# Kernel tuning notes

Hardware: AMD Instinct MI355X
Metric: run time of the kernel (lower is better)

The kernel has to match this reference:

```python
import jax, jax.numpy as jnp
import numpy as np

LN_EPS = 1e-5


def setup_inputs() -> dict:
    key = jax.random.key(0)
    k1, = jax.random.split(key, 1)
    B, C, H, W = 16, 512, 64, 64
    HW = H * W
    x = jax.random.normal(k1, (B, C, H, W), dtype=jnp.float32)
    gamma = jnp.ones((), dtype=jnp.float32)          # Scale(1) learnable scalar
    ln_weight = jnp.ones((HW,), dtype=jnp.float32)   # LayerNorm weight
    ln_bias = jnp.zeros((HW,), dtype=jnp.float32)    # LayerNorm bias
    return {"x": x, "gamma": gamma, "ln_weight": ln_weight, "ln_bias": ln_bias}


def reference(x, gamma, ln_weight, ln_bias):
    B, C, H, W = x.shape
    v = x.reshape(B, C, H * W)                       # [B, C, HW] (Q = K = V)
    energy = jnp.einsum('bcn,bdn->bcd', v, v)        # [B, C, C]
    attn = jax.nn.softmax(energy, axis=-1)
    out = jnp.einsum('bcd,bdn->bcn', attn, v)        # [B, C, HW]
    out = gamma * out + v                            # scale + residual
    # LayerNorm over last dim (HW), torch eps=1e-5
    mean = jnp.mean(out, axis=-1, keepdims=True)
    var = jnp.mean(jnp.square(out - mean), axis=-1, keepdims=True)
    out = (out - mean) * jax.lax.rsqrt(var + LN_EPS) * ln_weight + ln_bias
    return out.reshape(B, C, H, W)
```

## Files before the change

### kernel.cpp

```cpp
#include <hip/hip_runtime.h>
#include <hip/hip_bf16.h>

#define B_DIM 16
#define C_DIM 512
#define HW_DIM 4096
#define LN_EPS 1e-5f

using bf16 = __hip_bfloat16;
typedef __bf16 v8bf __attribute__((ext_vector_type(8)));
typedef float v4f __attribute__((ext_vector_type(4)));
typedef unsigned short v8us __attribute__((ext_vector_type(8)));
typedef unsigned short v4us __attribute__((ext_vector_type(4)));
using gptr_t = const __attribute__((address_space(1))) void*;
using lptr_t = __attribute__((address_space(3))) void*;

__device__ __forceinline__ unsigned short f2bf(float f) {
  unsigned int u = __float_as_uint(f);
  u = (u + 0x7fffu + ((u >> 16) & 1u)) >> 16;
  return (unsigned short)u;
}
__device__ __forceinline__ float bf2f(unsigned short us) {
  return __uint_as_float(((unsigned int)us) << 16);
}

__global__ __launch_bounds__(256) void k_convert_transpose(
    const float* __restrict__ x, unsigned short* __restrict__ v,
    unsigned short* __restrict__ vt) {
  __shared__ unsigned short tile[64 * 64];
  const int tid = threadIdx.x;
  const int b = blockIdx.z;
  const int n0 = blockIdx.x * 64;
  const int c0 = blockIdx.y * 64;
  const size_t boff = (size_t)b * ((size_t)C_DIM * HW_DIM);
  const float* xb = x + boff;
  unsigned short* vb = v + boff;
  unsigned short* vtb = vt + boff;

  const int cl = tid >> 3;
  const int hb = tid & 7;
  const int h8 = hb * 8;
#pragma unroll
  for (int j = 0; j < 2; ++j) {
    const int c = cl + j * 32;
    const float* src = xb + (size_t)(c0 + c) * HW_DIM + n0 + h8;
    const float4 f0 = ((const float4*)src)[0];
    const float4 f1 = ((const float4*)src)[1];
    v8us pack;
    pack[0] = f2bf(f0.x); pack[1] = f2bf(f0.y);
    pack[2] = f2bf(f0.z); pack[3] = f2bf(f0.w);
    pack[4] = f2bf(f1.x); pack[5] = f2bf(f1.y);
    pack[6] = f2bf(f1.z); pack[7] = f2bf(f1.w);
    *(v8us*)(vb + (size_t)(c0 + c) * HW_DIM + n0 + h8) = pack;
    const int key = (c & 7) ^ ((c >> 3) & 7);
    *(v8us*)(tile + c * 64 + ((hb ^ key) << 3)) = pack;
  }
  __syncthreads();
  const int nl = tid >> 3;
  const int c8 = (tid & 7) * 8;
  const int n = 2 * nl;
  v8us pa, pb;
#pragma unroll
  for (int e = 0; e < 8; ++e) {
    const int r = c8 + e;
    const int key = (r & 7) ^ ((r >> 3) & 7);
    const unsigned int w = *(const unsigned int*)(
        tile + r * 64 + (((n >> 3) ^ key) << 3) + (n & 7));
    pa[e] = (unsigned short)(w & 0xffffu);
    pb[e] = (unsigned short)(w >> 16);
  }
  *(v8us*)(vtb + (size_t)(n0 + n) * C_DIM + c0 + c8) = pa;
  *(v8us*)(vtb + (size_t)(n0 + n + 1) * C_DIM + c0 + c8) = pb;
}

__device__ __forceinline__ void stage_tiles(
    const bf16* __restrict__ a_base, const bf16* __restrict__ b_base,
    const int stride, const int k0, const int wave, const int lane,
    bf16* ldsA, bf16* ldsB) {
  const int srow = lane >> 3;
  const int skcol = (lane & 7) * 8;
#pragma unroll
  for (int i = 0; i < 4; ++i) {
    const int ci = wave * 4 + i;
    const int row = ci * 8 + srow;
    __builtin_amdgcn_global_load_lds(
        (gptr_t)(a_base + (size_t)row * stride + k0 + skcol),
        (lptr_t)(ldsA + ci * 512), 16, 0, 0);
    __builtin_amdgcn_global_load_lds(
        (gptr_t)(b_base + (size_t)row * stride + k0 + skcol),
        (lptr_t)(ldsB + ci * 512), 16, 0, 0);
  }
}

__device__ __forceinline__ void compute_tile(
    const bf16* ldsA, const bf16* ldsB, const int wave, const int lane,
    v4f acc[4][4]) {
  const int kb = (lane >> 4) * 8;
  const int rl = lane & 15;
  const int wr = wave >> 1, wc = wave & 1;
#pragma unroll
  for (int kk = 0; kk < 2; ++kk) {
    v8bf af[4], bfr[4];
#pragma unroll
    for (int m = 0; m < 4; ++m)
      af[m] = *(const v8bf*)(ldsA + (wr * 64 + m * 16 + rl) * 64 + kk * 32 + kb);
#pragma unroll
    for (int n = 0; n < 4; ++n)
      bfr[n] = *(const v8bf*)(ldsB + (wc * 64 + n * 16 + rl) * 64 + kk * 32 + kb);
#pragma unroll
    for (int m = 0; m < 4; ++m)
#pragma unroll
      for (int n = 0; n < 4; ++n)
        acc[m][n] = __builtin_amdgcn_mfma_f32_16x16x32_bf16(af[m], bfr[n], acc[m][n], 0, 0, 0);
  }
}

__device__ __forceinline__ void gemm_dbuf_loop(
    const bf16* __restrict__ a_base, const bf16* __restrict__ b_base,
    const int stride, const int ksteps, const int wave, const int lane,
    bf16* ldsA0, bf16* ldsB0, bf16* ldsA1, bf16* ldsB1, v4f acc[4][4]) {
  stage_tiles(a_base, b_base, stride, 0, wave, lane, ldsA0, ldsB0);
  __syncthreads();
  int cur = 0;
  for (int kt = 0; kt < ksteps - 1; ++kt) {
    if (cur == 0)
      stage_tiles(a_base, b_base, stride, (kt + 1) * 64, wave, lane, ldsA1, ldsB1);
    else
      stage_tiles(a_base, b_base, stride, (kt + 1) * 64, wave, lane, ldsA0, ldsB0);
    compute_tile(cur == 0 ? ldsA0 : ldsA1, cur == 0 ? ldsB0 : ldsB1, wave, lane, acc);
    __syncthreads();
    cur ^= 1;
  }
  compute_tile(cur == 0 ? ldsA0 : ldsA1, cur == 0 ? ldsB0 : ldsB1, wave, lane, acc);
}

__global__ __launch_bounds__(256) void k_gemm1(
    const bf16* __restrict__ v, float* __restrict__ e_part) {
  __shared__ __align__(16) bf16 lds[4][128 * 64];
  int t = blockIdx.x;
  const int ks = t >> 8;
  t &= 255;
  const int b = t >> 4;
  const int cb = (t >> 2) & 3;
  const int db = t & 3;
  const int tid = threadIdx.x;
  const int wave = tid >> 6, lane = tid & 63;
  const bf16* vb = v + (size_t)b * ((size_t)C_DIM * HW_DIM) + ks * (HW_DIM / 2);
  v4f acc[4][4] = {};
  gemm_dbuf_loop(vb + (size_t)(cb * 128) * HW_DIM,
                 vb + (size_t)(db * 128) * HW_DIM,
                 HW_DIM, (HW_DIM / 2) / 64, wave, lane,
                 lds[0], lds[1], lds[2], lds[3], acc);
  float* eb = e_part + (size_t)ks * ((size_t)B_DIM * C_DIM * C_DIM) +
              (size_t)b * (C_DIM * C_DIM);
  const int wr = wave >> 1, wc = wave & 1;
  const int rl = lane & 15;
  const int r0 = (lane >> 4) * 4;
#pragma unroll
  for (int m = 0; m < 4; ++m)
#pragma unroll
    for (int n = 0; n < 4; ++n) {
      const int row0 = cb * 128 + wr * 64 + m * 16 + r0;
      const int col = db * 128 + wc * 64 + n * 16 + rl;
#pragma unroll
      for (int r = 0; r < 4; ++r)
        eb[(size_t)(row0 + r) * C_DIM + col] = acc[m][n][r];
    }
}

__global__ __launch_bounds__(256) void k_softmax(
    const float* __restrict__ e_part, unsigned short* __restrict__ attn) {
  const int row = blockIdx.x;
  const float* e0 = e_part + (size_t)row * C_DIM;
  const float* e1 = e0 + (size_t)B_DIM * C_DIM * C_DIM;
  const int tid = threadIdx.x;
  const float v0 = e0[tid] + e1[tid];
  const float v1 = e0[tid + 256] + e1[tid + 256];
  float mx = fmaxf(v0, v1);
#pragma unroll
  for (int off = 32; off > 0; off >>= 1) mx = fmaxf(mx, __shfl_xor(mx, off));
  __shared__ float rmax[4], rsum[4];
  const int wv = tid >> 6, ln = tid & 63;
  if (ln == 0) rmax[wv] = mx;
  __syncthreads();
  mx = fmaxf(fmaxf(rmax[0], rmax[1]), fmaxf(rmax[2], rmax[3]));
  const float p0 = __expf(v0 - mx), p1 = __expf(v1 - mx);
  float s = p0 + p1;
#pragma unroll
  for (int off = 32; off > 0; off >>= 1) s += __shfl_xor(s, off);
  if (ln == 0) rsum[wv] = s;
  __syncthreads();
  s = rsum[0] + rsum[1] + rsum[2] + rsum[3];
  const float inv = 1.0f / s;
  attn[(size_t)row * C_DIM + tid] = f2bf(p0 * inv);
  attn[(size_t)row * C_DIM + tid + 256] = f2bf(p1 * inv);
}

#define TILE_E (256 * 64)

__device__ __forceinline__ void stage_half8(
    const bf16* __restrict__ g, bf16* l, int k0, int wave, int lane) {
  const int lrow = lane >> 3, lc = lane & 7;
#pragma unroll
  for (int i = 0; i < 2; ++i) {
    const int row = i * 64 + wave * 8 + lrow;
    __builtin_amdgcn_global_load_lds(
        (gptr_t)(g + (size_t)row * C_DIM + k0 + ((lc ^ (row & 7)) << 3)),
        (lptr_t)(l + (i * 64 + wave * 8) * 64), 16, 0, 0);
  }
}
__device__ __forceinline__ void stage_op2(
    const bf16* __restrict__ g, bf16* l, int k0, int wave, int lane) {
  stage_half8(g, l, k0, wave, lane);
  stage_half8(g + (size_t)128 * C_DIM, l + 128 * 64, k0, wave, lane);
}
__device__ __forceinline__ v8bf ld_frag8(const bf16* l, int row, int j) {
  return *(const v8bf*)(l + row * 64 + ((j ^ (row & 7)) << 3));
}

__global__ __launch_bounds__(512, 2) void k_gemm2(
    const bf16* __restrict__ attn, const bf16* __restrict__ vt,
    float* __restrict__ out) {
  __shared__ __align__(16) bf16 smem[4 * TILE_E];
  const int bid = blockIdx.x;
  const int t = (bid & 7) * 64 + (bid >> 3);
  const int b = t >> 5;
  const int cb = (t >> 4) & 1;
  const int nb = t & 15;
  const int tid = threadIdx.x;
  const int wave = tid >> 6, lane = tid & 63;
  const int wm = wave >> 2, wn = wave & 3;
  const int rl = lane & 15, kq = lane >> 4;

  const bf16* Ab = attn + (size_t)b * (C_DIM * C_DIM) + (size_t)(cb * 256) * C_DIM;
  const bf16* Bb = vt + (size_t)b * ((size_t)C_DIM * HW_DIM) + (size_t)(nb * 256) * C_DIM;

  v4f acc[8][4] = {};

  stage_op2(Bb, smem + 2 * TILE_E, 0, wave, lane);
  stage_op2(Ab, smem, 0, wave, lane);
  stage_op2(Bb, smem + 3 * TILE_E, 64, wave, lane);
  stage_op2(Ab, smem + TILE_E, 64, wave, lane);
  asm volatile("s_waitcnt vmcnt(8)" ::: "memory");
  __builtin_amdgcn_s_barrier();

  v8bf a[4][2], b01[2][2], b23[2][2];
  for (int kt = 0; kt < 8; ++kt) {
    const bf16* LA = smem + (kt & 1) * TILE_E;
    const bf16* LB = smem + (2 + (kt & 1)) * TILE_E;
    bf16* SA = smem + (kt & 1) * TILE_E;
    bf16* SB = smem + (2 + (kt & 1)) * TILE_E;
#pragma unroll
    for (int mi = 0; mi < 4; ++mi)
#pragma unroll
      for (int kk = 0; kk < 2; ++kk)
        a[mi][kk] = ld_frag8(LA, wm * 128 + mi * 16 + rl, kk * 4 + kq);
#pragma unroll
    for (int ni = 0; ni < 2; ++ni)
#pragma unroll
      for (int kk = 0; kk < 2; ++kk)
        b01[ni][kk] = ld_frag8(LB, wn * 64 + ni * 16 + rl, kk * 4 + kq);
    __builtin_amdgcn_s_barrier();
    asm volatile("s_waitcnt lgkmcnt(0)");
    __builtin_amdgcn_s_setprio(1);
#pragma unroll
    for (int kk = 0; kk < 2; ++kk)
#pragma unroll
      for (int mi = 0; mi < 4; ++mi)
#pragma unroll
        for (int ni = 0; ni < 2; ++ni)
          acc[mi][ni] = __builtin_amdgcn_mfma_f32_16x16x32_bf16(
              a[mi][kk], b01[ni][kk], acc[mi][ni], 0, 0, 0);
    __builtin_amdgcn_s_setprio(0);
    __builtin_amdgcn_s_barrier();
#pragma unroll
    for (int ni = 0; ni < 2; ++ni)
#pragma unroll
      for (int kk = 0; kk < 2; ++kk)
        b23[ni][kk] = ld_frag8(LB, wn * 64 + (ni + 2) * 16 + rl, kk * 4 + kq);
    __builtin_amdgcn_s_barrier();
    asm volatile("s_waitcnt lgkmcnt(0)");
    __builtin_amdgcn_s_setprio(1);
#pragma unroll
    for (int kk = 0; kk < 2; ++kk)
#pragma unroll
      for (int mi = 0; mi < 4; ++mi)
#pragma unroll
        for (int ni = 0; ni < 2; ++ni)
          acc[mi][ni + 2] = __builtin_amdgcn_mfma_f32_16x16x32_bf16(
              a[mi][kk], b23[ni][kk], acc[mi][ni + 2], 0, 0, 0);
    __builtin_amdgcn_s_setprio(0);
    __builtin_amdgcn_s_barrier();
#pragma unroll
    for (int mi = 0; mi < 4; ++mi)
#pragma unroll
      for (int kk = 0; kk < 2; ++kk)
        a[mi][kk] = ld_frag8(LA, wm * 128 + (mi + 4) * 16 + rl, kk * 4 + kq);
    if (kt < 6) stage_op2(Bb, SB, (kt + 2) * 64, wave, lane);
    __builtin_amdgcn_s_barrier();
    asm volatile("s_waitcnt lgkmcnt(0)");
    __builtin_amdgcn_s_setprio(1);
#pragma unroll
    for (int kk = 0; kk < 2; ++kk)
#pragma unroll
      for (int mi = 0; mi < 4; ++mi)
#pragma unroll
        for (int ni = 0; ni < 2; ++ni)
          acc[mi + 4][ni + 2] = __builtin_amdgcn_mfma_f32_16x16x32_bf16(
              a[mi][kk], b23[ni][kk], acc[mi + 4][ni + 2], 0, 0, 0);
    __builtin_amdgcn_s_setprio(0);
    __builtin_amdgcn_s_barrier();
    if (kt < 6) stage_op2(Ab, SA, (kt + 2) * 64, wave, lane);
    __builtin_amdgcn_s_barrier();
    __builtin_amdgcn_s_setprio(1);
#pragma unroll
    for (int kk = 0; kk < 2; ++kk)
#pragma unroll
      for (int mi = 0; mi < 4; ++mi)
#pragma unroll
        for (int ni = 0; ni < 2; ++ni)
          acc[mi + 4][ni] = __builtin_amdgcn_mfma_f32_16x16x32_bf16(
              a[mi][kk], b01[ni][kk], acc[mi + 4][ni], 0, 0, 0);
    __builtin_amdgcn_s_setprio(0);
    if (kt < 6)
      asm volatile("s_waitcnt vmcnt(8)" ::: "memory");
    else if (kt == 6)
      asm volatile("s_waitcnt vmcnt(0)" ::: "memory");
    __builtin_amdgcn_s_barrier();
  }

  float* smf = (float*)smem;
  float* ob = out + (size_t)b * ((size_t)C_DIM * HW_DIM) +
              (size_t)(cb * 256) * HW_DIM + nb * 256;
#pragma unroll
  for (int h = 0; h < 2; ++h) {
    if (wm == h) {
#pragma unroll
      for (int mi = 0; mi < 8; ++mi)
#pragma unroll
        for (int ni = 0; ni < 4; ++ni)
#pragma unroll
          for (int rr = 0; rr < 4; ++rr) {
            const int rloc = mi * 16 + kq * 4 + rr;
            const int col = wn * 64 + ni * 16 + rl;
            const int key = rloc & 7;
            smf[rloc * 256 + ((((col >> 2) ^ key) << 2) | (col & 3))] =
                acc[mi][ni][rr];
          }
    }
    __syncthreads();
#pragma unroll
    for (int it = 0; it < 16; ++it) {
      const int rloc = it * 8 + wave;
      const float4 vv =
          *(const float4*)(smf + rloc * 256 + ((lane ^ (rloc & 7)) << 2));
      *(float4*)(ob + (size_t)(h * 128 + rloc) * HW_DIM + lane * 4) = vv;
    }
    __syncthreads();
  }
}

__global__ __launch_bounds__(256) void k_ln(
    float* __restrict__ out, const unsigned short* __restrict__ vres,
    const float* __restrict__ gamma, const float* __restrict__ w,
    const float* __restrict__ bias) {
  const int row = blockIdx.x;
  float* p = out + (size_t)row * HW_DIM;
  const unsigned short* vr = vres + (size_t)row * HW_DIM;
  const float g = gamma[0];
  const int tid = threadIdx.x;
  float4 vals[4];
  float s = 0.f, ss = 0.f;
#pragma unroll
  for (int i = 0; i < 4; ++i) {
    const int idx = tid + i * 256;
    const float4 av = ((const float4*)p)[idx];
    const v4us rv = *(const v4us*)(vr + idx * 4);
    float4 vv;
    vv.x = g * av.x + bf2f(rv[0]);
    vv.y = g * av.y + bf2f(rv[1]);
    vv.z = g * av.z + bf2f(rv[2]);
    vv.w = g * av.w + bf2f(rv[3]);
    vals[i] = vv;
    s += vv.x + vv.y + vv.z + vv.w;
    ss += vv.x * vv.x + vv.y * vv.y + vv.z * vv.z + vv.w * vv.w;
  }
#pragma unroll
  for (int off = 32; off > 0; off >>= 1) {
    s += __shfl_xor(s, off);
    ss += __shfl_xor(ss, off);
  }
  __shared__ float rs[4], rss[4];
  const int wv = tid >> 6, ln = tid & 63;
  if (ln == 0) { rs[wv] = s; rss[wv] = ss; }
  __syncthreads();
  s = rs[0] + rs[1] + rs[2] + rs[3];
  ss = rss[0] + rss[1] + rss[2] + rss[3];
  const float mean = s * (1.f / HW_DIM);
  const float var = ss * (1.f / HW_DIM) - mean * mean;
  const float rstd = rsqrtf(var + LN_EPS);
#pragma unroll
  for (int i = 0; i < 4; ++i) {
    const int idx = tid + i * 256;
    const float4 vv = vals[i];
    const float4 w4 = ((const float4*)w)[idx];
    const float4 b4 = ((const float4*)bias)[idx];
    float4 r;
    r.x = (vv.x - mean) * rstd * w4.x + b4.x;
    r.y = (vv.y - mean) * rstd * w4.y + b4.y;
    r.z = (vv.z - mean) * rstd * w4.z + b4.z;
    r.w = (vv.w - mean) * rstd * w4.w + b4.w;
    ((float4*)p)[idx] = r;
  }
}

extern "C" void kernel_launch(void* const* d_in, const int* in_sizes, int n_in,
                              void* d_out, int out_size, void* d_ws, size_t ws_size,
                              hipStream_t stream) {
  const float* x = (const float*)d_in[0];
  const float* gamma = (const float*)d_in[1];
  const float* lnw = (const float*)d_in[2];
  const float* lnb = (const float*)d_in[3];
  float* out = (float*)d_out;
  char* ws = (char*)d_ws;

  const size_t n_elem = (size_t)B_DIM * C_DIM * HW_DIM;
  const size_t e_elems = (size_t)B_DIM * C_DIM * C_DIM;
  unsigned short* vbf = (unsigned short*)ws;
  unsigned short* vbfT = (unsigned short*)(ws + 2 * n_elem);
  float* e_part = (float*)(ws + 4 * n_elem);
  unsigned short* attn =
      (unsigned short*)(ws + 4 * n_elem + 2 * e_elems * sizeof(float));

  k_convert_transpose<<<dim3(HW_DIM / 64, C_DIM / 64, B_DIM), 256, 0, stream>>>(
      x, vbf, vbfT);
  k_gemm1<<<512, 256, 0, stream>>>((const bf16*)vbf, e_part);
  k_softmax<<<B_DIM * C_DIM, 256, 0, stream>>>(e_part, attn);
  k_gemm2<<<512, 512, 0, stream>>>((const bf16*)attn, (const bf16*)vbfT, out);
  k_ln<<<B_DIM * C_DIM, 256, 0, stream>>>(out, vbf, gamma, lnw, lnb);
}
```

Measured before the change: 231.6 us.

## Reuse 256x256 eight-phase GEMM for energy and split convert from transpose

The energy GEMM moves from 128x128 tiles with a 2-way K split to the 256x256, 512-thread, eight-phase pipelined loop already used by gemm2, now generalised with stride parameters and run with a 4-way K split. A swizzled LDS-bounce epilogue is shared by both GEMMs. Softmax sums four partials and writes attention in place over the partial buffer using a doubled row stride. The fused convert+transpose is split into a streaming convert kernel and a separate transpose that rereads the bf16 data, adding an extra launch and extra traffic.

```diff
diff --git a/kernel.cpp b/kernel.cpp
--- a/kernel.cpp
+++ b/kernel.cpp
@@ -5,6 +5,7 @@
 #define C_DIM 512
 #define HW_DIM 4096
 #define LN_EPS 1e-5f
+#define ATTN_STRIDE 1024
 
 using bf16 = __hip_bfloat16;
 typedef __bf16 v8bf __attribute__((ext_vector_type(8)));
@@ -23,34 +24,41 @@
   return __uint_as_float(((unsigned int)us) << 16);
 }
 
-__global__ __launch_bounds__(256) void k_convert_transpose(
-    const float* __restrict__ x, unsigned short* __restrict__ v,
-    unsigned short* __restrict__ vt) {
-  __shared__ unsigned short tile[64 * 64];
-  const int tid = threadIdx.x;
-  const int b = blockIdx.z;
-  const int n0 = blockIdx.x * 64;
-  const int c0 = blockIdx.y * 64;
-  const size_t boff = (size_t)b * ((size_t)C_DIM * HW_DIM);
-  const float* xb = x + boff;
-  unsigned short* vb = v + boff;
-  unsigned short* vtb = vt + boff;
-
-  const int cl = tid >> 3;
-  const int hb = tid & 7;
-  const int h8 = hb * 8;
-#pragma unroll
-  for (int j = 0; j < 2; ++j) {
-    const int c = cl + j * 32;
-    const float* src = xb + (size_t)(c0 + c) * HW_DIM + n0 + h8;
-    const float4 f0 = ((const float4*)src)[0];
-    const float4 f1 = ((const float4*)src)[1];
+__global__ __launch_bounds__(256) void k_convert(
+    const float* __restrict__ x, unsigned short* __restrict__ v) {
+  const size_t i0 = ((size_t)blockIdx.x * 256 + threadIdx.x) * 8;
+  const size_t step = (size_t)2048 * 256 * 8;
+#pragma unroll
+  for (int it = 0; it < 8; ++it) {
+    const size_t base = i0 + (size_t)it * step;
+    const float4 f0 = ((const float4*)(x + base))[0];
+    const float4 f1 = ((const float4*)(x + base))[1];
     v8us pack;
     pack[0] = f2bf(f0.x); pack[1] = f2bf(f0.y);
     pack[2] = f2bf(f0.z); pack[3] = f2bf(f0.w);
     pack[4] = f2bf(f1.x); pack[5] = f2bf(f1.y);
     pack[6] = f2bf(f1.z); pack[7] = f2bf(f1.w);
-    *(v8us*)(vb + (size_t)(c0 + c) * HW_DIM + n0 + h8) = pack;
+    *(v8us*)(v + base) = pack;
+  }
+}
+
+__global__ __launch_bounds__(256) void k_transpose(
+    const unsigned short* __restrict__ v, unsigned short* __restrict__ vt) {
+  __shared__ unsigned short tile[64 * 64];
+  const int tid = threadIdx.x;
+  const int b = blockIdx.z;
+  const int n0 = blockIdx.x * 64;
+  const int c0 = blockIdx.y * 64;
+  const size_t boff = (size_t)b * ((size_t)C_DIM * HW_DIM);
+  const unsigned short* vb = v + boff;
+  unsigned short* vtb = vt + boff;
+
+  const int cl = tid >> 3;
+  const int hb = tid & 7;
+#pragma unroll
+  for (int j = 0; j < 2; ++j) {
+    const int c = cl + j * 32;
+    const v8us pack = *(const v8us*)(vb + (size_t)(c0 + c) * HW_DIM + n0 + hb * 8);
     const int key = (c & 7) ^ ((c >> 3) & 7);
     *(v8us*)(tile + c * 64 + ((hb ^ key) << 3)) = pack;
   }
@@ -72,109 +80,198 @@
   *(v8us*)(vtb + (size_t)(n0 + n + 1) * C_DIM + c0 + c8) = pb;
 }
 
-__device__ __forceinline__ void stage_tiles(
-    const bf16* __restrict__ a_base, const bf16* __restrict__ b_base,
-    const int stride, const int k0, const int wave, const int lane,
-    bf16* ldsA, bf16* ldsB) {
-  const int srow = lane >> 3;
-  const int skcol = (lane & 7) * 8;
-#pragma unroll
-  for (int i = 0; i < 4; ++i) {
-    const int ci = wave * 4 + i;
-    const int row = ci * 8 + srow;
+#define TILE_E (256 * 64)
+
+__device__ __forceinline__ void stage_half8(
+    const bf16* __restrict__ g, bf16* l, int k0, int stride, int wave, int lane) {
+  const int lrow = lane >> 3, lc = lane & 7;
+#pragma unroll
+  for (int i = 0; i < 2; ++i) {
+    const int row = i * 64 + wave * 8 + lrow;
     __builtin_amdgcn_global_load_lds(
-        (gptr_t)(a_base + (size_t)row * stride + k0 + skcol),
-        (lptr_t)(ldsA + ci * 512), 16, 0, 0);
-    __builtin_amdgcn_global_load_lds(
-        (gptr_t)(b_base + (size_t)row * stride + k0 + skcol),
-        (lptr_t)(ldsB + ci * 512), 16, 0, 0);
-  }
-}
-
-__device__ __forceinline__ void compute_tile(
-    const bf16* ldsA, const bf16* ldsB, const int wave, const int lane,
-    v4f acc[4][4]) {
-  const int kb = (lane >> 4) * 8;
-  const int rl = lane & 15;
-  const int wr = wave >> 1, wc = wave & 1;
-#pragma unroll
-  for (int kk = 0; kk < 2; ++kk) {
-    v8bf af[4], bfr[4];
-#pragma unroll
-    for (int m = 0; m < 4; ++m)
-      af[m] = *(const v8bf*)(ldsA + (wr * 64 + m * 16 + rl) * 64 + kk * 32 + kb);
-#pragma unroll
-    for (int n = 0; n < 4; ++n)
-      bfr[n] = *(const v8bf*)(ldsB + (wc * 64 + n * 16 + rl) * 64 + kk * 32 + kb);
-#pragma unroll
-    for (int m = 0; m < 4; ++m)
-#pragma unroll
-      for (int n = 0; n < 4; ++n)
-        acc[m][n] = __builtin_amdgcn_mfma_f32_16x16x32_bf16(af[m], bfr[n], acc[m][n], 0, 0, 0);
-  }
-}
-
-__device__ __forceinline__ void gemm_dbuf_loop(
-    const bf16* __restrict__ a_base, const bf16* __restrict__ b_base,
-    const int stride, const int ksteps, const int wave, const int lane,
-    bf16* ldsA0, bf16* ldsB0, bf16* ldsA1, bf16* ldsB1, v4f acc[4][4]) {
-  stage_tiles(a_base, b_base, stride, 0, wave, lane, ldsA0, ldsB0);
-  __syncthreads();
-  int cur = 0;
-  for (int kt = 0; kt < ksteps - 1; ++kt) {
-    if (cur == 0)
-      stage_tiles(a_base, b_base, stride, (kt + 1) * 64, wave, lane, ldsA1, ldsB1);
-    else
-      stage_tiles(a_base, b_base, stride, (kt + 1) * 64, wave, lane, ldsA0, ldsB0);
-    compute_tile(cur == 0 ? ldsA0 : ldsA1, cur == 0 ? ldsB0 : ldsB1, wave, lane, acc);
+        (gptr_t)(g + (size_t)row * stride + k0 + ((lc ^ (row & 7)) << 3)),
+        (lptr_t)(l + (i * 64 + wave * 8) * 64), 16, 0, 0);
+  }
+}
+__device__ __forceinline__ void stage_op2(
+    const bf16* __restrict__ g, bf16* l, int k0, int stride, int wave, int lane) {
+  stage_half8(g, l, k0, stride, wave, lane);
+  stage_half8(g + (size_t)128 * stride, l + 128 * 64, k0, stride, wave, lane);
+}
+__device__ __forceinline__ v8bf ld_frag8(const bf16* l, int row, int j) {
+  return *(const v8bf*)(l + row * 64 + ((j ^ (row & 7)) << 3));
+}
+
+__device__ __forceinline__ void gemm_8ph_loop(
+    const bf16* __restrict__ Ab, const bf16* __restrict__ Bb,
+    const int strideA, const int strideB, const int kts,
+    bf16* smem, const int wave, const int lane, v4f acc[8][4]) {
+  const int wm = wave >> 2, wn = wave & 3;
+  const int rl = lane & 15, kq = lane >> 4;
+
+  stage_op2(Bb, smem + 2 * TILE_E, 0, strideB, wave, lane);
+  stage_op2(Ab, smem, 0, strideA, wave, lane);
+  stage_op2(Bb, smem + 3 * TILE_E, 64, strideB, wave, lane);
+  stage_op2(Ab, smem + TILE_E, 64, strideA, wave, lane);
+  asm volatile("s_waitcnt vmcnt(8)" ::: "memory");
+  __builtin_amdgcn_s_barrier();
+
+  v8bf a[4][2], b01[2][2], b23[2][2];
+  for (int kt = 0; kt < kts; ++kt) {
+    const bf16* LA = smem + (kt & 1) * TILE_E;
+    const bf16* LB = smem + (2 + (kt & 1)) * TILE_E;
+    bf16* SA = smem + (kt & 1) * TILE_E;
+    bf16* SB = smem + (2 + (kt & 1)) * TILE_E;
+#pragma unroll
+    for (int mi = 0; mi < 4; ++mi)
+#pragma unroll
+      for (int kk = 0; kk < 2; ++kk)
+        a[mi][kk] = ld_frag8(LA, wm * 128 + mi * 16 + rl, kk * 4 + kq);
+#pragma unroll
+    for (int ni = 0; ni < 2; ++ni)
+#pragma unroll
+      for (int kk = 0; kk < 2; ++kk)
+        b01[ni][kk] = ld_frag8(LB, wn * 64 + ni * 16 + rl, kk * 4 + kq);
+    __builtin_amdgcn_s_barrier();
+    asm volatile("s_waitcnt lgkmcnt(0)");
+    __builtin_amdgcn_s_setprio(1);
+#pragma unroll
+    for (int kk = 0; kk < 2; ++kk)
+#pragma unroll
+      for (int mi = 0; mi < 4; ++mi)
+#pragma unroll
+        for (int ni = 0; ni < 2; ++ni)
+          acc[mi][ni] = __builtin_amdgcn_mfma_f32_16x16x32_bf16(
+              a[mi][kk], b01[ni][kk], acc[mi][ni], 0, 0, 0);
+    __builtin_amdgcn_s_setprio(0);
+    __builtin_amdgcn_s_barrier();
+#pragma unroll
+    for (int ni = 0; ni < 2; ++ni)
+#pragma unroll
+      for (int kk = 0; kk < 2; ++kk)
+        b23[ni][kk] = ld_frag8(LB, wn * 64 + (ni + 2) * 16 + rl, kk * 4 + kq);
+    __builtin_amdgcn_s_barrier();
+    asm volatile("s_waitcnt lgkmcnt(0)");
+    __builtin_amdgcn_s_setprio(1);
+#pragma unroll
+    for (int kk = 0; kk < 2; ++kk)
+#pragma unroll
+      for (int mi = 0; mi < 4; ++mi)
+#pragma unroll
+        for (int ni = 0; ni < 2; ++ni)
+          acc[mi][ni + 2] = __builtin_amdgcn_mfma_f32_16x16x32_bf16(
+              a[mi][kk], b23[ni][kk], acc[mi][ni + 2], 0, 0, 0);
+    __builtin_amdgcn_s_setprio(0);
+    __builtin_amdgcn_s_barrier();
+#pragma unroll
+    for (int mi = 0; mi < 4; ++mi)
+#pragma unroll
+      for (int kk = 0; kk < 2; ++kk)
+        a[mi][kk] = ld_frag8(LA, wm * 128 + (mi + 4) * 16 + rl, kk * 4 + kq);
+    if (kt < kts - 2) stage_op2(Bb, SB, (kt + 2) * 64, strideB, wave, lane);
+    __builtin_amdgcn_s_barrier();
+    asm volatile("s_waitcnt lgkmcnt(0)");
+    __builtin_amdgcn_s_setprio(1);
+#pragma unroll
+    for (int kk = 0; kk < 2; ++kk)
+#pragma unroll
+      for (int mi = 0; mi < 4; ++mi)
+#pragma unroll
+        for (int ni = 0; ni < 2; ++ni)
+          acc[mi + 4][ni + 2] = __builtin_amdgcn_mfma_f32_16x16x32_bf16(
+              a[mi][kk], b23[ni][kk], acc[mi + 4][ni + 2], 0, 0, 0);
+    __builtin_amdgcn_s_setprio(0);
+    __builtin_amdgcn_s_barrier();
+    if (kt < kts - 2) stage_op2(Ab, SA, (kt + 2) * 64, strideA, wave, lane);
+    __builtin_amdgcn_s_barrier();
+    __builtin_amdgcn_s_setprio(1);
+#pragma unroll
+    for (int kk = 0; kk < 2; ++kk)
+#pragma unroll
+      for (int mi = 0; mi < 4; ++mi)
+#pragma unroll
+        for (int ni = 0; ni < 2; ++ni)
+          acc[mi + 4][ni] = __builtin_amdgcn_mfma_f32_16x16x32_bf16(
+              a[mi][kk], b01[ni][kk], acc[mi + 4][ni], 0, 0, 0);
+    __builtin_amdgcn_s_setprio(0);
+    if (kt < kts - 2)
+      asm volatile("s_waitcnt vmcnt(8)" ::: "memory");
+    else if (kt == kts - 2)
+      asm volatile("s_waitcnt vmcnt(0)" ::: "memory");
+    __builtin_amdgcn_s_barrier();
+  }
+}
+
+__device__ __forceinline__ void epilogue_bounce(
+    v4f acc[8][4], bf16* smem, float* ob, const int out_stride,
+    const int wave, const int lane) {
+  const int wm = wave >> 2, wn = wave & 3;
+  const int rl = lane & 15, kq = lane >> 4;
+  float* smf = (float*)smem;
+#pragma unroll
+  for (int h = 0; h < 2; ++h) {
+    if (wm == h) {
+#pragma unroll
+      for (int mi = 0; mi < 8; ++mi)
+#pragma unroll
+        for (int ni = 0; ni < 4; ++ni)
+#pragma unroll
+          for (int rr = 0; rr < 4; ++rr) {
+            const int rloc = mi * 16 + kq * 4 + rr;
+            const int col = wn * 64 + ni * 16 + rl;
+            const int key = rloc & 7;
+            smf[rloc * 256 + ((((col >> 2) ^ key) << 2) | (col & 3))] =
+                acc[mi][ni][rr];
+          }
+    }
     __syncthreads();
-    cur ^= 1;
-  }
-  compute_tile(cur == 0 ? ldsA0 : ldsA1, cur == 0 ? ldsB0 : ldsB1, wave, lane, acc);
-}
-
-__global__ __launch_bounds__(256) void k_gemm1(
+#pragma unroll
+    for (int it = 0; it < 16; ++it) {
+      const int rloc = it * 8 + wave;
+      const float4 vv =
+          *(const float4*)(smf + rloc * 256 + ((lane ^ (rloc & 7)) << 2));
+      *(float4*)(ob + (size_t)(h * 128 + rloc) * out_stride + lane * 4) = vv;
+    }
+    __syncthreads();
+  }
+}
+
+__global__ __launch_bounds__(512, 2) void k_gemm1(
     const bf16* __restrict__ v, float* __restrict__ e_part) {
-  __shared__ __align__(16) bf16 lds[4][128 * 64];
-  int t = blockIdx.x;
-  const int ks = t >> 8;
-  t &= 255;
+  __shared__ __align__(16) bf16 smem[4 * TILE_E];
+  const int bid = blockIdx.x;
+  const int t = (bid & 7) * 32 + (bid >> 3);
+  const int ks = t & 3;
+  const int db = (t >> 2) & 1;
+  const int cb = (t >> 3) & 1;
   const int b = t >> 4;
-  const int cb = (t >> 2) & 3;
-  const int db = t & 3;
   const int tid = threadIdx.x;
   const int wave = tid >> 6, lane = tid & 63;
-  const bf16* vb = v + (size_t)b * ((size_t)C_DIM * HW_DIM) + ks * (HW_DIM / 2);
-  v4f acc[4][4] = {};
-  gemm_dbuf_loop(vb + (size_t)(cb * 128) * HW_DIM,
-                 vb + (size_t)(db * 128) * HW_DIM,
-                 HW_DIM, (HW_DIM / 2) / 64, wave, lane,
-                 lds[0], lds[1], lds[2], lds[3], acc);
-  float* eb = e_part + (size_t)ks * ((size_t)B_DIM * C_DIM * C_DIM) +
-              (size_t)b * (C_DIM * C_DIM);
-  const int wr = wave >> 1, wc = wave & 1;
-  const int rl = lane & 15;
-  const int r0 = (lane >> 4) * 4;
-#pragma unroll
-  for (int m = 0; m < 4; ++m)
-#pragma unroll
-    for (int n = 0; n < 4; ++n) {
-      const int row0 = cb * 128 + wr * 64 + m * 16 + r0;
-      const int col = db * 128 + wc * 64 + n * 16 + rl;
-#pragma unroll
-      for (int r = 0; r < 4; ++r)
-        eb[(size_t)(row0 + r) * C_DIM + col] = acc[m][n][r];
-    }
+
+  const bf16* vb = v + (size_t)b * ((size_t)C_DIM * HW_DIM) + ks * 1024;
+  const bf16* Ab = vb + (size_t)(cb * 256) * HW_DIM;
+  const bf16* Bb = vb + (size_t)(db * 256) * HW_DIM;
+
+  v4f acc[8][4] = {};
+  gemm_8ph_loop(Ab, Bb, HW_DIM, HW_DIM, 16, smem, wave, lane, acc);
+
+  float* ob = e_part + (size_t)ks * ((size_t)B_DIM * C_DIM * C_DIM) +
+              (size_t)b * (C_DIM * C_DIM) + (size_t)(cb * 256) * C_DIM + db * 256;
+  epilogue_bounce(acc, smem, ob, C_DIM, wave, lane);
 }
 
 __global__ __launch_bounds__(256) void k_softmax(
     const float* __restrict__ e_part, unsigned short* __restrict__ attn) {
   const int row = blockIdx.x;
+  const size_t bcc = (size_t)B_DIM * C_DIM * C_DIM;
   const float* e0 = e_part + (size_t)row * C_DIM;
-  const float* e1 = e0 + (size_t)B_DIM * C_DIM * C_DIM;
-  const int tid = threadIdx.x;
-  const float v0 = e0[tid] + e1[tid];
-  const float v1 = e0[tid + 256] + e1[tid + 256];
+  const int tid = threadIdx.x;
+  float v0 = 0.f, v1 = 0.f;
+#pragma unroll
+  for (int p = 0; p < 4; ++p) {
+    v0 += e0[p * bcc + tid];
+    v1 += e0[p * bcc + tid + 256];
+  }
   float mx = fmaxf(v0, v1);
 #pragma unroll
   for (int off = 32; off > 0; off >>= 1) mx = fmaxf(mx, __shfl_xor(mx, off));
@@ -191,30 +288,8 @@
   __syncthreads();
   s = rsum[0] + rsum[1] + rsum[2] + rsum[3];
   const float inv = 1.0f / s;
-  attn[(size_t)row * C_DIM + tid] = f2bf(p0 * inv);
-  attn[(size_t)row * C_DIM + tid + 256] = f2bf(p1 * inv);
-}
-
-#define TILE_E (256 * 64)
-
-__device__ __forceinline__ void stage_half8(
-    const bf16* __restrict__ g, bf16* l, int k0, int wave, int lane) {
-  const int lrow = lane >> 3, lc = lane & 7;
-#pragma unroll
-  for (int i = 0; i < 2; ++i) {
-    const int row = i * 64 + wave * 8 + lrow;
-    __builtin_amdgcn_global_load_lds(
-        (gptr_t)(g + (size_t)row * C_DIM + k0 + ((lc ^ (row & 7)) << 3)),
-        (lptr_t)(l + (i * 64 + wave * 8) * 64), 16, 0, 0);
-  }
-}
-__device__ __forceinline__ void stage_op2(
-    const bf16* __restrict__ g, bf16* l, int k0, int wave, int lane) {
-  stage_half8(g, l, k0, wave, lane);
-  stage_half8(g + (size_t)128 * C_DIM, l + 128 * 64, k0, wave, lane);
-}
-__device__ __forceinline__ v8bf ld_frag8(const bf16* l, int row, int j) {
-  return *(const v8bf*)(l + row * 64 + ((j ^ (row & 7)) << 3));
+  attn[(size_t)row * ATTN_STRIDE + tid] = f2bf(p0 * inv);
+  attn[(size_t)row * ATTN_STRIDE + tid + 256] = f2bf(p1 * inv);
 }
 
 __global__ __launch_bounds__(512, 2) void k_gemm2(
@@ -228,135 +303,17 @@
   const int nb = t & 15;
   const int tid = threadIdx.x;
   const int wave = tid >> 6, lane = tid & 63;
-  const int wm = wave >> 2, wn = wave & 3;
-  const int rl = lane & 15, kq = lane >> 4;
-
-  const bf16* Ab = attn + (size_t)b * (C_DIM * C_DIM) + (size_t)(cb * 256) * C_DIM;
-  const bf16* Bb = vt + (size_t)b * ((size_t)C_DIM * HW_DIM) + (size_t)(nb * 256) * C_DIM;
+
+  const bf16* Ab = attn + (size_t)(b * C_DIM + cb * 256) * ATTN_STRIDE;
+  const bf16* Bb = vt + (size_t)b * ((size_t)C_DIM * HW_DIM) +
+                   (size_t)(nb * 256) * C_DIM;
 
   v4f acc[8][4] = {};
-
-  stage_op2(Bb, smem + 2 * TILE_E, 0, wave, lane);
-  stage_op2(Ab, smem, 0, wave, lane);
-  stage_op2(Bb, smem + 3 * TILE_E, 64, wave, lane);
-  stage_op2(Ab, smem + TILE_E, 64, wave, lane);
-  asm volatile("s_waitcnt vmcnt(8)" ::: "memory");
-  __builtin_amdgcn_s_barrier();
-
-  v8bf a[4][2], b01[2][2], b23[2][2];
-  for (int kt = 0; kt < 8; ++kt) {
-    const bf16* LA = smem + (kt & 1) * TILE_E;
-    const bf16* LB = smem + (2 + (kt & 1)) * TILE_E;
-    bf16* SA = smem + (kt & 1) * TILE_E;
-    bf16* SB = smem + (2 + (kt & 1)) * TILE_E;
-#pragma unroll
-    for (int mi = 0; mi < 4; ++mi)
-#pragma unroll
-      for (int kk = 0; kk < 2; ++kk)
-        a[mi][kk] = ld_frag8(LA, wm * 128 + mi * 16 + rl, kk * 4 + kq);
-#pragma unroll
-    for (int ni = 0; ni < 2; ++ni)
-#pragma unroll
-      for (int kk = 0; kk < 2; ++kk)
-        b01[ni][kk] = ld_frag8(LB, wn * 64 + ni * 16 + rl, kk * 4 + kq);
-    __builtin_amdgcn_s_barrier();
-    asm volatile("s_waitcnt lgkmcnt(0)");
-    __builtin_amdgcn_s_setprio(1);
-#pragma unroll
-    for (int kk = 0; kk < 2; ++kk)
-#pragma unroll
-      for (int mi = 0; mi < 4; ++mi)
-#pragma unroll
-        for (int ni = 0; ni < 2; ++ni)
-          acc[mi][ni] = __builtin_amdgcn_mfma_f32_16x16x32_bf16(
-              a[mi][kk], b01[ni][kk], acc[mi][ni], 0, 0, 0);
-    __builtin_amdgcn_s_setprio(0);
-    __builtin_amdgcn_s_barrier();
-#pragma unroll
-    for (int ni = 0; ni < 2; ++ni)
-#pragma unroll
-      for (int kk = 0; kk < 2; ++kk)
-        b23[ni][kk] = ld_frag8(LB, wn * 64 + (ni + 2) * 16 + rl, kk * 4 + kq);
-    __builtin_amdgcn_s_barrier();
-    asm volatile("s_waitcnt lgkmcnt(0)");
-    __builtin_amdgcn_s_setprio(1);
-#pragma unroll
-    for (int kk = 0; kk < 2; ++kk)
-#pragma unroll
-      for (int mi = 0; mi < 4; ++mi)
-#pragma unroll
-        for (int ni = 0; ni < 2; ++ni)
-          acc[mi][ni + 2] = __builtin_amdgcn_mfma_f32_16x16x32_bf16(
-              a[mi][kk], b23[ni][kk], acc[mi][ni + 2], 0, 0, 0);
-    __builtin_amdgcn_s_setprio(0);
-    __builtin_amdgcn_s_barrier();
-#pragma unroll
-    for (int mi = 0; mi < 4; ++mi)
-#pragma unroll
-      for (int kk = 0; kk < 2; ++kk)
-        a[mi][kk] = ld_frag8(LA, wm * 128 + (mi + 4) * 16 + rl, kk * 4 + kq);
-    if (kt < 6) stage_op2(Bb, SB, (kt + 2) * 64, wave, lane);
-    __builtin_amdgcn_s_barrier();
-    asm volatile("s_waitcnt lgkmcnt(0)");
-    __builtin_amdgcn_s_setprio(1);
-#pragma unroll
-    for (int kk = 0; kk < 2; ++kk)
-#pragma unroll
-      for (int mi = 0; mi < 4; ++mi)
-#pragma unroll
-        for (int ni = 0; ni < 2; ++ni)
-          acc[mi + 4][ni + 2] = __builtin_amdgcn_mfma_f32_16x16x32_bf16(
-              a[mi][kk], b23[ni][kk], acc[mi + 4][ni + 2], 0, 0, 0);
-    __builtin_amdgcn_s_setprio(0);
-    __builtin_amdgcn_s_barrier();
-    if (kt < 6) stage_op2(Ab, SA, (kt + 2) * 64, wave, lane);
-    __builtin_amdgcn_s_barrier();
-    __builtin_amdgcn_s_setprio(1);
-#pragma unroll
-    for (int kk = 0; kk < 2; ++kk)
-#pragma unroll
-      for (int mi = 0; mi < 4; ++mi)
-#pragma unroll
-        for (int ni = 0; ni < 2; ++ni)
-          acc[mi + 4][ni] = __builtin_amdgcn_mfma_f32_16x16x32_bf16(
-              a[mi][kk], b01[ni][kk], acc[mi + 4][ni], 0, 0, 0);
-    __builtin_amdgcn_s_setprio(0);
-    if (kt < 6)
-      asm volatile("s_waitcnt vmcnt(8)" ::: "memory");
-    else if (kt == 6)
-      asm volatile("s_waitcnt vmcnt(0)" ::: "memory");
-    __builtin_amdgcn_s_barrier();
-  }
-
-  float* smf = (float*)smem;
+  gemm_8ph_loop(Ab, Bb, ATTN_STRIDE, C_DIM, 8, smem, wave, lane, acc);
+
   float* ob = out + (size_t)b * ((size_t)C_DIM * HW_DIM) +
               (size_t)(cb * 256) * HW_DIM + nb * 256;
-#pragma unroll
-  for (int h = 0; h < 2; ++h) {
-    if (wm == h) {
-#pragma unroll
-      for (int mi = 0; mi < 8; ++mi)
-#pragma unroll
-        for (int ni = 0; ni < 4; ++ni)
-#pragma unroll
-          for (int rr = 0; rr < 4; ++rr) {
-            const int rloc = mi * 16 + kq * 4 + rr;
-            const int col = wn * 64 + ni * 16 + rl;
-            const int key = rloc & 7;
-            smf[rloc * 256 + ((((col >> 2) ^ key) << 2) | (col & 3))] =
-                acc[mi][ni][rr];
-          }
-    }
-    __syncthreads();
-#pragma unroll
-    for (int it = 0; it < 16; ++it) {
-      const int rloc = it * 8 + wave;
-      const float4 vv =
-          *(const float4*)(smf + rloc * 256 + ((lane ^ (rloc & 7)) << 2));
-      *(float4*)(ob + (size_t)(h * 128 + rloc) * HW_DIM + lane * 4) = vv;
-    }
-    __syncthreads();
-  }
+  epilogue_bounce(acc, smem, ob, HW_DIM, wave, lane);
 }
 
 __global__ __launch_bounds__(256) void k_ln(
@@ -424,16 +381,15 @@
   char* ws = (char*)d_ws;
 
   const size_t n_elem = (size_t)B_DIM * C_DIM * HW_DIM;
-  const size_t e_elems = (size_t)B_DIM * C_DIM * C_DIM;
   unsigned short* vbf = (unsigned short*)ws;
   unsigned short* vbfT = (unsigned short*)(ws + 2 * n_elem);
   float* e_part = (float*)(ws + 4 * n_elem);
-  unsigned short* attn =
-      (unsigned short*)(ws + 4 * n_elem + 2 * e_elems * sizeof(float));
-
-  k_convert_transpose<<<dim3(HW_DIM / 64, C_DIM / 64, B_DIM), 256, 0, stream>>>(
-      x, vbf, vbfT);
-  k_gemm1<<<512, 256, 0, stream>>>((const bf16*)vbf, e_part);
+  unsigned short* attn = (unsigned short*)e_part;
+
+  k_convert<<<2048, 256, 0, stream>>>(x, vbf);
+  k_transpose<<<dim3(HW_DIM / 64, C_DIM / 64, B_DIM), 256, 0, stream>>>(
+      vbf, vbfT);
+  k_gemm1<<<256, 512, 0, stream>>>((const bf16*)vbf, e_part);
   k_softmax<<<B_DIM * C_DIM, 256, 0, stream>>>(e_part, attn);
   k_gemm2<<<512, 512, 0, stream>>>((const bf16*)attn, (const bf16*)vbfT, out);
   k_ln<<<B_DIM * C_DIM, 256, 0, stream>>>(out, vbf, gamma, lnw, lnb);
```

Measured after the change: 238.1 us. 1.03x slower.
